# Kernel tuning notes

Measured on AMD Instinct MI355X. Metric: run time of the kernel, lower is better.

## Reference

```python
import jax, jax.numpy as jnp
import numpy as np

N = 50000
E = 600000
D = 128


def setup_inputs() -> dict:
    key = jax.random.key(0)
    ks = jax.random.split(key, 6)
    x = jax.random.normal(ks[0], (N, D), dtype=jnp.float32)
    src = jax.random.randint(ks[1], (E,), 0, N, dtype=jnp.int32)
    dst = jax.random.randint(ks[2], (E,), 0, N, dtype=jnp.int32)
    W = jax.random.normal(ks[3], (D, D), dtype=jnp.float32) * (1.0 / np.sqrt(D))
    b = jax.random.normal(ks[4], (D,), dtype=jnp.float32) * 0.01
    root_emb = jax.random.normal(ks[5], (1, D), dtype=jnp.float32)
    return {"x": x, "src": src, "dst": dst, "W": W, "b": b, "root_emb": root_emb}


def reference(x, src, dst, W, b, root_emb):
    # h = Linear(x)
    h = x @ W.T + b  # (N, D)
    # in-degree (count of incoming edges per node) + 1 for self loop
    deg = jax.ops.segment_sum(jnp.ones((E,), dtype=jnp.float32), dst, num_segments=N) + 1.0  # (N,)
    deg_inv_sqrt = deg ** -0.5  # deg >= 1, no inf
    # per-edge symmetric norm
    norm = deg_inv_sqrt[src] * deg_inv_sqrt[dst]  # (E,)
    # message: norm * relu(h_src), scatter-sum to dst
    m = norm[:, None] * jax.nn.relu(h[src])  # (E, D)
    agg = jax.ops.segment_sum(m, dst, num_segments=N)  # (N, D)
    # self loop term
    self_loop = jax.nn.relu(h + root_emb) * (1.0 / deg)[:, None]
    return agg + self_loop
```

## Files before the change

### kernel.cpp

```cpp
#include <hip/hip_runtime.h>

#define DD 128

typedef _Float16 h8 __attribute__((ext_vector_type(8)));
typedef float f4 __attribute__((ext_vector_type(4)));

__global__ __launch_bounds__(256) void prep(const float* __restrict__ W,
    _Float16* __restrict__ Wh, int* __restrict__ cnt, int N) {
  const int gid = blockIdx.x * blockDim.x + threadIdx.x;
  const int stride = gridDim.x * blockDim.x;
  for (int i = gid; i < DD * DD; i += stride) Wh[i] = (_Float16)W[i];
  for (int i = gid; i < N; i += stride) cnt[i] = 0;
}

__global__ __launch_bounds__(256) void gemm_mfma(const float* __restrict__ x,
    const _Float16* __restrict__ Wh, const float* __restrict__ bias,
    _Float16* __restrict__ h16, const int* __restrict__ dst,
    int* __restrict__ cnt, int* __restrict__ slot, int E, int N) {
  __shared__ __align__(16) char lds[32768 + 32768 + 4096];
  const int tid = threadIdx.x;
  const int gid = blockIdx.x * 256 + tid;
  const int gsz = gridDim.x * 256;
  for (int e = gid; e < E; e += gsz) slot[e] = atomicAdd(cnt + dst[e], 1);

  const int lane = tid & 63;
  const int w    = tid >> 6;
  const int lrow = lane & 15;
  const int srow = (lane >> 4) << 2;
  const int row0 = blockIdx.x * 64;

#pragma unroll
  for (int i = 0; i < 8; ++i) {
    const char* s = (const char*)Wh + i * 4096 + tid * 16;
    __builtin_amdgcn_global_load_lds(
        (const __attribute__((address_space(1))) void*)s,
        (__attribute__((address_space(3))) void*)(lds + 32768 + i * 4096 + ((tid >> 6) << 10)),
        16, 0, 0);
  }
#pragma unroll
  for (int i = 0; i < 8; ++i) {
    const int ol = i * 4096 + tid * 16;
    const int r  = ol >> 9;
    const int cg = (ol >> 4) & 31;
    int grow = row0 + r; if (grow >= N) grow = N - 1;
    const char* s = (const char*)x + (size_t)grow * 512 + ((cg ^ (r & 7)) << 4);
    __builtin_amdgcn_global_load_lds(
        (const __attribute__((address_space(1))) void*)s,
        (__attribute__((address_space(3))) void*)(lds + i * 4096 + ((tid >> 6) << 10)),
        16, 0, 0);
  }
  __syncthreads();

  h8 wb[2][4];
  float bj[2];
#pragma unroll
  for (int jt = 0; jt < 2; ++jt) {
    const int col = w * 32 + jt * 16 + lrow;
    bj[jt] = bias[col];
#pragma unroll
    for (int ks = 0; ks < 4; ++ks)
      wb[jt][ks] = *(const h8*)(lds + 32768 + col * 256 + ks * 64 + (lane >> 4) * 16);
  }

  _Float16* cs = (_Float16*)(lds + 65536);
#pragma unroll
  for (int rt = 0; rt < 4; ++rt) {
    const int rowbase = row0 + rt * 16;
    if (rowbase >= N) break;
    f4 acc[2] = {(f4){0.f,0.f,0.f,0.f}, (f4){0.f,0.f,0.f,0.f}};
#pragma unroll
    for (int ks = 0; ks < 4; ++ks) {
      const int r   = rt * 16 + lrow;
      const int cg0 = ks * 8 + (lane >> 4) * 2;
      const f4 a0 = *(const f4*)(lds + r * 512 + ((cg0 ^ (r & 7)) << 4));
      const f4 a1 = *(const f4*)(lds + r * 512 + (((cg0 + 1) ^ (r & 7)) << 4));
      h8 af;
      af[0]=(_Float16)a0.x; af[1]=(_Float16)a0.y; af[2]=(_Float16)a0.z; af[3]=(_Float16)a0.w;
      af[4]=(_Float16)a1.x; af[5]=(_Float16)a1.y; af[6]=(_Float16)a1.z; af[7]=(_Float16)a1.w;
      acc[0] = __builtin_amdgcn_mfma_f32_16x16x32_f16(af, wb[0][ks], acc[0], 0, 0, 0);
      acc[1] = __builtin_amdgcn_mfma_f32_16x16x32_f16(af, wb[1][ks], acc[1], 0, 0, 0);
    }
#pragma unroll
    for (int jt = 0; jt < 2; ++jt)
#pragma unroll
      for (int r = 0; r < 4; ++r)
        cs[(srow + r) * DD + w * 32 + jt * 16 + lrow] = (_Float16)(acc[jt][r] + bj[jt]);
    __syncthreads();
    const int frow = rowbase + (tid >> 4);
    if (frow < N) {
      const f4 v = *(const f4*)((char*)cs + tid * 16);
      *(f4*)((char*)h16 + (size_t)frow * 256 + (tid & 15) * 16) = v;
    }
    __syncthreads();
  }
}

__global__ __launch_bounds__(256) void scan1(const int* __restrict__ cnt,
    int* __restrict__ rowptr, int* __restrict__ bsum, float* __restrict__ dis, int N) {
  __shared__ int s[256];
  const int tid = threadIdx.x;
  const int idx = blockIdx.x * 1024 + tid * 4;
  int4 v = {0, 0, 0, 0};
  if (idx + 3 < N) v = *(const int4*)(cnt + idx);
  else {
    if (idx + 0 < N) v.x = cnt[idx];
    if (idx + 1 < N) v.y = cnt[idx + 1];
    if (idx + 2 < N) v.z = cnt[idx + 2];
  }
  if (idx + 0 < N) dis[idx + 0] = rsqrtf((float)(v.x + 1));
  if (idx + 1 < N) dis[idx + 1] = rsqrtf((float)(v.y + 1));
  if (idx + 2 < N) dis[idx + 2] = rsqrtf((float)(v.z + 1));
  if (idx + 3 < N) dis[idx + 3] = rsqrtf((float)(v.w + 1));
  const int mysum = v.x + v.y + v.z + v.w;
  s[tid] = mysum;
  __syncthreads();
  for (int off = 1; off < 256; off <<= 1) {
    int t = (tid >= off) ? s[tid - off] : 0;
    __syncthreads();
    s[tid] += t;
    __syncthreads();
  }
  if (tid == 255) bsum[blockIdx.x] = s[255];
  int p = s[tid] - mysum;
  if (idx + 0 < N) rowptr[idx + 0] = p; p += v.x;
  if (idx + 1 < N) rowptr[idx + 1] = p; p += v.y;
  if (idx + 2 < N) rowptr[idx + 2] = p; p += v.z;
  if (idx + 3 < N) rowptr[idx + 3] = p;
}

__global__ __launch_bounds__(256) void scan2(const int* __restrict__ bsum,
    int* __restrict__ boff, int* __restrict__ rowptr, int nb, int N) {
  __shared__ int s[256];
  const int tid = threadIdx.x;
  const int v = (tid < nb) ? bsum[tid] : 0;
  s[tid] = v;
  __syncthreads();
  for (int off = 1; off < 256; off <<= 1) {
    int t = (tid >= off) ? s[tid - off] : 0;
    __syncthreads();
    s[tid] += t;
    __syncthreads();
  }
  if (tid < nb) boff[tid] = s[tid] - v;
  if (tid == nb - 1) rowptr[N] = v;
}

__global__ void fill_csr(const int* __restrict__ src, const int* __restrict__ dst,
    const int* __restrict__ rowptr, const int* __restrict__ boff,
    const int* __restrict__ slot, int* __restrict__ esrc, int E) {
  int e = blockIdx.x * blockDim.x + threadIdx.x;
  if (e < E) {
    const int t = dst[e];
    esrc[rowptr[t] + boff[t >> 10] + slot[e]] = src[e];
  }
}

__global__ __launch_bounds__(256) void csr_agg(const int* __restrict__ esrc,
    const int* __restrict__ rowptr, const int* __restrict__ boff,
    const _Float16* __restrict__ h16, const float* __restrict__ dis,
    const float* __restrict__ root, float* __restrict__ out, int N) {
  int gid = blockIdx.x * blockDim.x + threadIdx.x;
  if (gid >= N * 16) return;
  const int n = gid >> 4, q = gid & 15;
  const float dt  = dis[n];
  const float inv = dt * dt;
  const h8* hv8 = reinterpret_cast<const h8*>(h16);
  const f4 r0 = reinterpret_cast<const f4*>(root)[q * 2];
  const f4 r1 = reinterpret_cast<const f4*>(root)[q * 2 + 1];
  const h8 hv = hv8[n * 16 + q];
  float acc[8];
  acc[0] = fmaxf((float)hv[0] + r0.x, 0.0f) * inv;
  acc[1] = fmaxf((float)hv[1] + r0.y, 0.0f) * inv;
  acc[2] = fmaxf((float)hv[2] + r0.z, 0.0f) * inv;
  acc[3] = fmaxf((float)hv[3] + r0.w, 0.0f) * inv;
  acc[4] = fmaxf((float)hv[4] + r1.x, 0.0f) * inv;
  acc[5] = fmaxf((float)hv[5] + r1.y, 0.0f) * inv;
  acc[6] = fmaxf((float)hv[6] + r1.z, 0.0f) * inv;
  acc[7] = fmaxf((float)hv[7] + r1.w, 0.0f) * inv;
  float ea[8] = {0.f, 0.f, 0.f, 0.f, 0.f, 0.f, 0.f, 0.f};
  const int beg = rowptr[n] + boff[n >> 10];
  const int end = rowptr[n + 1] + boff[(n + 1) >> 10];
  int k = beg;
  for (; k + 3 < end; k += 4) {
    const int s0 = esrc[k], s1 = esrc[k + 1], s2 = esrc[k + 2], s3 = esrc[k + 3];
    const float w0 = dis[s0], w1 = dis[s1], w2 = dis[s2], w3 = dis[s3];
    const h8 g0 = hv8[s0 * 16 + q];
    const h8 g1 = hv8[s1 * 16 + q];
    const h8 g2 = hv8[s2 * 16 + q];
    const h8 g3 = hv8[s3 * 16 + q];
#pragma unroll
    for (int j = 0; j < 8; ++j)
      ea[j] += fmaxf((float)g0[j], 0.0f) * w0 + fmaxf((float)g1[j], 0.0f) * w1
             + fmaxf((float)g2[j], 0.0f) * w2 + fmaxf((float)g3[j], 0.0f) * w3;
  }
  for (; k < end; ++k) {
    const int s0 = esrc[k];
    const float w0 = dis[s0];
    const h8 g0 = hv8[s0 * 16 + q];
#pragma unroll
    for (int j = 0; j < 8; ++j) ea[j] += fmaxf((float)g0[j], 0.0f) * w0;
  }
  f4 o0, o1;
  o0.x = acc[0] + ea[0] * dt; o0.y = acc[1] + ea[1] * dt;
  o0.z = acc[2] + ea[2] * dt; o0.w = acc[3] + ea[3] * dt;
  o1.x = acc[4] + ea[4] * dt; o1.y = acc[5] + ea[5] * dt;
  o1.z = acc[6] + ea[6] * dt; o1.w = acc[7] + ea[7] * dt;
  reinterpret_cast<f4*>(out)[n * 32 + q * 2]     = o0;
  reinterpret_cast<f4*>(out)[n * 32 + q * 2 + 1] = o1;
}

extern "C" void kernel_launch(void* const* d_in, const int* in_sizes, int n_in,
                              void* d_out, int out_size, void* d_ws, size_t ws_size,
                              hipStream_t stream) {
  const float* x    = (const float*)d_in[0];
  const int*   src  = (const int*)d_in[1];
  const int*   dst  = (const int*)d_in[2];
  const float* W    = (const float*)d_in[3];
  const float* bias = (const float*)d_in[4];
  const float* root = (const float*)d_in[5];
  float* out = (float*)d_out;
  const int N = in_sizes[0] / DD;
  const int E = in_sizes[1];

  char* ws = (char*)d_ws;
  size_t off = 0;
  _Float16* h16 = (_Float16*)(ws + off); off += (size_t)N * DD * 2;
  int*   cnt    = (int*)  (ws + off); off += (size_t)N * 4;
  float* dis    = (float*)(ws + off); off += (size_t)N * 4;
  int*   rowptr = (int*)  (ws + off); off += (size_t)(N + 2) * 4;
  int*   esrc   = (int*)  (ws + off); off += (size_t)E * 4;
  int*   slot   = (int*)  (ws + off); off += (size_t)E * 4;
  int*   bsum   = (int*)  (ws + off); off += 256 * 4;
  int*   boff   = (int*)  (ws + off); off += 256 * 4;
  _Float16* Wh  = (_Float16*)(ws + off); off += (size_t)DD * DD * 2;

  const int nb  = (N + 1023) / 1024;
  const int nbt = (N + 63) / 64;
  prep<<<128, 256, 0, stream>>>(W, Wh, cnt, N);
  gemm_mfma<<<nbt, 256, 0, stream>>>(x, Wh, bias, h16, dst, cnt, slot, E, N);
  scan1<<<nb, 256, 0, stream>>>(cnt, rowptr, bsum, dis, N);
  scan2<<<1, 256, 0, stream>>>(bsum, boff, rowptr, nb, N);
  fill_csr<<<(E + 255) / 256, 256, 0, stream>>>(src, dst, rowptr, boff, slot, esrc, E);
  csr_agg<<<(N * 16 + 255) / 256, 256, 0, stream>>>(esrc, rowptr, boff, h16, dis, root, out, N);
}
```

Baseline: 86.83 us.

## Fold block-offset scan into consumers and vectorize CSR fill

```diff
diff --git a/kernel.cpp b/kernel.cpp
--- a/kernel.cpp
+++ b/kernel.cpp
@@ -128,38 +128,54 @@
   if (idx + 3 < N) rowptr[idx + 3] = p;
 }
 
-__global__ __launch_bounds__(256) void scan2(const int* __restrict__ bsum,
-    int* __restrict__ boff, int* __restrict__ rowptr, int nb, int N) {
-  __shared__ int s[256];
-  const int tid = threadIdx.x;
-  const int v = (tid < nb) ? bsum[tid] : 0;
-  s[tid] = v;
+__device__ __forceinline__ void boff_scan(const int* __restrict__ bsum,
+    int* __restrict__ sbof, int tid, int nb) {
+  if (tid < 64) {
+    const int v = (tid < nb) ? bsum[tid] : 0;
+    int incl = v;
+#pragma unroll
+    for (int off = 1; off < 64; off <<= 1) {
+      const int t = __shfl_up(incl, off);
+      if (tid >= off) incl += t;
+    }
+    sbof[tid] = incl - v;
+  }
   __syncthreads();
-  for (int off = 1; off < 256; off <<= 1) {
-    int t = (tid >= off) ? s[tid - off] : 0;
-    __syncthreads();
-    s[tid] += t;
-    __syncthreads();
-  }
-  if (tid < nb) boff[tid] = s[tid] - v;
-  if (tid == nb - 1) rowptr[N] = v;
-}
-
-__global__ void fill_csr(const int* __restrict__ src, const int* __restrict__ dst,
-    const int* __restrict__ rowptr, const int* __restrict__ boff,
-    const int* __restrict__ slot, int* __restrict__ esrc, int E) {
-  int e = blockIdx.x * blockDim.x + threadIdx.x;
-  if (e < E) {
-    const int t = dst[e];
-    esrc[rowptr[t] + boff[t >> 10] + slot[e]] = src[e];
+}
+
+__global__ __launch_bounds__(256) void fill_csr(const int* __restrict__ src,
+    const int* __restrict__ dst, const int* __restrict__ rowptr,
+    const int* __restrict__ bsum, const int* __restrict__ slot,
+    int* __restrict__ esrc, int E, int nb) {
+  __shared__ int sbof[64];
+  const int tid = threadIdx.x;
+  boff_scan(bsum, sbof, tid, nb);
+  const int e4 = blockIdx.x * 256 + tid;
+  const int e  = e4 * 4;
+  if (e + 3 < E) {
+    const int4 s4 = ((const int4*)src)[e4];
+    const int4 d4 = ((const int4*)dst)[e4];
+    const int4 l4 = ((const int4*)slot)[e4];
+    esrc[rowptr[d4.x] + sbof[d4.x >> 10] + l4.x] = s4.x;
+    esrc[rowptr[d4.y] + sbof[d4.y >> 10] + l4.y] = s4.y;
+    esrc[rowptr[d4.z] + sbof[d4.z >> 10] + l4.z] = s4.z;
+    esrc[rowptr[d4.w] + sbof[d4.w >> 10] + l4.w] = s4.w;
+  } else if (e < E) {
+    for (int i = e; i < E; ++i) {
+      const int t = dst[i];
+      esrc[rowptr[t] + sbof[t >> 10] + slot[i]] = src[i];
+    }
   }
 }
 
 __global__ __launch_bounds__(256) void csr_agg(const int* __restrict__ esrc,
-    const int* __restrict__ rowptr, const int* __restrict__ boff,
+    const int* __restrict__ rowptr, const int* __restrict__ bsum,
     const _Float16* __restrict__ h16, const float* __restrict__ dis,
-    const float* __restrict__ root, float* __restrict__ out, int N) {
-  int gid = blockIdx.x * blockDim.x + threadIdx.x;
+    const float* __restrict__ root, float* __restrict__ out, int N, int E, int nb) {
+  __shared__ int sbof[64];
+  const int tid = threadIdx.x;
+  boff_scan(bsum, sbof, tid, nb);
+  int gid = blockIdx.x * 256 + tid;
   if (gid >= N * 16) return;
   const int n = gid >> 4, q = gid & 15;
   const float dt  = dis[n];
@@ -178,8 +194,8 @@
   acc[6] = fmaxf((float)hv[6] + r1.z, 0.0f) * inv;
   acc[7] = fmaxf((float)hv[7] + r1.w, 0.0f) * inv;
   float ea[8] = {0.f, 0.f, 0.f, 0.f, 0.f, 0.f, 0.f, 0.f};
-  const int beg = rowptr[n] + boff[n >> 10];
-  const int end = rowptr[n + 1] + boff[(n + 1) >> 10];
+  const int beg = rowptr[n] + sbof[n >> 10];
+  const int end = (n == N - 1) ? E : rowptr[n + 1] + sbof[(n + 1) >> 10];
   int k = beg;
   for (; k + 3 < end; k += 4) {
     const int s0 = esrc[k], s1 = esrc[k + 1], s2 = esrc[k + 2], s3 = esrc[k + 3];
@@ -231,7 +247,6 @@
   int*   esrc   = (int*)  (ws + off); off += (size_t)E * 4;
   int*   slot   = (int*)  (ws + off); off += (size_t)E * 4;
   int*   bsum   = (int*)  (ws + off); off += 256 * 4;
-  int*   boff   = (int*)  (ws + off); off += 256 * 4;
   _Float16* Wh  = (_Float16*)(ws + off); off += (size_t)DD * DD * 2;
 
   const int nb  = (N + 1023) / 1024;
@@ -239,7 +254,6 @@
   prep<<<128, 256, 0, stream>>>(W, Wh, cnt, N);
   gemm_mfma<<<nbt, 256, 0, stream>>>(x, Wh, bias, h16, dst, cnt, slot, E, N);
   scan1<<<nb, 256, 0, stream>>>(cnt, rowptr, bsum, dis, N);
-  scan2<<<1, 256, 0, stream>>>(bsum, boff, rowptr, nb, N);
-  fill_csr<<<(E + 255) / 256, 256, 0, stream>>>(src, dst, rowptr, boff, slot, esrc, E);
-  csr_agg<<<(N * 16 + 255) / 256, 256, 0, stream>>>(esrc, rowptr, boff, h16, dis, root, out, N);
-}
+  fill_csr<<<((E + 3) / 4 + 255) / 256, 256, 0, stream>>>(src, dst, rowptr, bsum, slot, esrc, E, nb);
+  csr_agg<<<(N * 16 + 255) / 256, 256, 0, stream>>>(esrc, rowptr, bsum, h16, dis, root, out, N, E, nb);
+}
```

Result: no change. 86.14 us (median of 2 runs) (-0.8%).
